# Kernel optimization log

Hardware: AMD Instinct MI355X
Metric: run time of the kernel (lower is better)

## Reference

```python
import jax, jax.numpy as jnp
import numpy as np

D = 128

def setup_inputs() -> dict:
    key = jax.random.key(0)
    k1, k2, k3, k4, k5, k6, k7 = jax.random.split(key, 7)
    B, L = 2048, 200
    target = jax.random.normal(k1, (B, D), dtype=jnp.float32)
    item_seq = jax.random.normal(k2, (B, L, D), dtype=jnp.float32)
    seq_len = jax.random.randint(k3, (B,), 0, 200, dtype=jnp.int64 if jax.config.jax_enable_x64 else jnp.int32)
    # MLP params: Linear(4D -> 2D), Linear(2D -> 1), PyTorch-style init scale
    s1 = 1.0 / np.sqrt(4 * D)
    s2 = 1.0 / np.sqrt(2 * D)
    W1 = jax.random.uniform(k4, (4 * D, 2 * D), minval=-s1, maxval=s1, dtype=jnp.float32)
    b1 = jax.random.uniform(k5, (2 * D,), minval=-s1, maxval=s1, dtype=jnp.float32)
    W2 = jax.random.uniform(k6, (2 * D, 1), minval=-s2, maxval=s2, dtype=jnp.float32)
    b2 = jax.random.uniform(k7, (1,), minval=-s2, maxval=s2, dtype=jnp.float32)
    return {"target": target, "item_seq": item_seq, "seq_len": seq_len,
            "W1": W1, "b1": b1, "W2": W2, "b2": b2}

def reference(target, item_seq, seq_len, W1, b1, W2, b2):
    B, L, Dd = item_seq.shape
    t = target[:, None, :]                              # B 1 D (broadcast over L)
    tgt = jnp.broadcast_to(t, (B, L, Dd))
    sub = item_seq - tgt
    dot = item_seq * tgt
    mlp_in = jnp.concatenate([tgt, item_seq, sub, dot], axis=-1)   # B L 4D
    h = jax.nn.relu(jnp.einsum('blf,fh->blh', mlp_in, W1) + b1)    # B L 2D
    score = jnp.einsum('blh,ho->blo', h, W2) + b2                  # B L 1
    mask = (jnp.arange(L)[None, :] < seq_len[:, None]).astype(item_seq.dtype)  # B L
    weighted = score * item_seq * mask[:, :, None]                 # B L D
    return jnp.sum(weighted, axis=1)                               # B D
```

## Files before the change

### kernel.cpp

```cpp
#include <hip/hip_runtime.h>
#include <hip/hip_bf16.h>

typedef short short8 __attribute__((ext_vector_type(8)));
typedef float f32x4 __attribute__((ext_vector_type(4)));

#define XS 136

static __device__ inline short f2bf(float f) {
    unsigned u = __float_as_uint(f);
    unsigned r = (u + 0x7fffu + ((u >> 16) & 1u)) >> 16;
    return (short)r;
}
static __device__ inline float bf2f(short s) {
    return __uint_as_float(((unsigned)(unsigned short)s) << 16);
}

__global__ void prep(const float* __restrict__ W1, short* __restrict__ Wbc,
                     short* __restrict__ Wd) {
    int idx = blockIdx.x * 256 + threadIdx.x;
    int half = idx >> 15;
    int i = idx & 32767;
    int j = i & 7;
    int l = (i >> 3) & 63;
    int s = (i >> 9) & 3;
    int t = i >> 11;
    int k = s * 32 + ((l >> 4) << 3) + j;
    int n = t * 16 + (l & 15);
    if (half == 0) Wbc[i] = f2bf(W1[(128 + k) * 256 + n] + W1[(256 + k) * 256 + n]);
    else           Wd[i]  = f2bf(W1[(384 + k) * 256 + n]);
}

__global__ void compute_u(const float* __restrict__ target, const float* __restrict__ W1,
                          const float* __restrict__ b1, float* __restrict__ U) {
    const int b8 = blockIdx.x;
    const int tid = threadIdx.x;
    __shared__ float tl[1024];
#pragma unroll
    for (int k = 0; k < 4; k++) tl[k * 256 + tid] = target[b8 * 1024 + k * 256 + tid];
    __syncthreads();
    float acc[8] = {0.f, 0.f, 0.f, 0.f, 0.f, 0.f, 0.f, 0.f};
#pragma unroll 8
    for (int d = 0; d < 128; ++d) {
        float wud = W1[d * 256 + tid] - W1[(256 + d) * 256 + tid];
#pragma unroll
        for (int r = 0; r < 8; r++) acc[r] += tl[r * 128 + d] * wud;
    }
    float bj = b1[tid];
#pragma unroll
    for (int r = 0; r < 8; r++) U[(b8 * 8 + r) * 256 + tid] = acc[r] + bj;
}

__launch_bounds__(256, 2)
__global__ void din_main(const float* __restrict__ target, const float* __restrict__ item_seq,
                         const int* __restrict__ seq_len, const float* __restrict__ W2,
                         const float* __restrict__ b2p, const short* __restrict__ Wbc,
                         const short* __restrict__ Wd, const float* __restrict__ U,
                         float* __restrict__ out) {
    const int b = blockIdx.x;
    const int tid = threadIdx.x;
    const int lane = tid & 63;
    const int w = tid >> 6;
    const int col = lane & 15;
    const int q = lane >> 4;

    const int slen = seq_len[b];
    const int nt = (slen + 15) >> 4;

    __shared__ __attribute__((aligned(16))) short Xl[2][16 * XS];
    __shared__ __attribute__((aligned(16))) float tsh[128];
    __shared__ float u_s[256];
    __shared__ float w2_s[256];
    __shared__ __attribute__((aligned(16))) float scoreP[16][4];
    __shared__ float out_s[128];

    const int r = tid >> 4;
    const int c = (tid & 15) << 3;

    float4 v0, v1;
    {
        const float4* src = (const float4*)(item_seq + (((size_t)b * 200 + r) * 128 + c));
        v0 = src[0]; v1 = src[1];
    }

    if (tid < 128) tsh[tid] = target[b * 128 + tid];
    u_s[tid] = U[b * 256 + tid];
    w2_s[tid] = W2[tid];
    const float b2 = b2p[0];
    __syncthreads();

    short8 bfrag[4][4];
#pragma unroll
    for (int s = 0; s < 4; s++) {
        const float4* tp = (const float4*)(tsh + s * 32 + q * 8);
        float4 ta = tp[0], tb = tp[1];
        float tk[8] = {ta.x, ta.y, ta.z, ta.w, tb.x, tb.y, tb.z, tb.w};
#pragma unroll
        for (int i = 0; i < 4; i++) {
            size_t off = ((size_t)((w * 4 + i) * 4 + s) * 64 + lane) * 8;
            short8 bc = *(const short8*)(Wbc + off);
            short8 dd = *(const short8*)(Wd + off);
            short8 e;
#pragma unroll
            for (int j = 0; j < 8; j++) e[j] = f2bf(bf2f(bc[j]) + tk[j] * bf2f(dd[j]));
            bfrag[i][s] = e;
        }
    }

    float u_c[4], w2c[4];
#pragma unroll
    for (int i = 0; i < 4; i++) {
        int j = (w * 4 + i) * 16 + col;
        u_c[i] = u_s[j];
        w2c[i] = w2_s[j];
    }

    const int d = tid & 127;
    const int g = tid >> 7;
    float out_val = 0.f;
    f32x4 acc[4];

    for (int mt = 0; mt < nt; ++mt) {
        const int l0 = mt * 16;
        short* xb = Xl[mt & 1];

        {
            float v[8] = {v0.x, v0.y, v0.z, v0.w, v1.x, v1.y, v1.z, v1.w};
            short8 p;
#pragma unroll
            for (int j = 0; j < 8; j++) p[j] = f2bf(v[j]);
            *(short8*)(xb + r * XS + c) = p;
        }
        __syncthreads();

        if (mt + 1 < nt) {
            int lr = l0 + 16 + r;
            if (lr > 199) lr = 199;
            const float4* src = (const float4*)(item_seq + (((size_t)b * 200 + lr) * 128 + c));
            v0 = src[0]; v1 = src[1];
        }

#pragma unroll
        for (int i = 0; i < 4; i++) acc[i] = (f32x4){0.f, 0.f, 0.f, 0.f};
        const short* arow = xb + col * XS + q * 8;
#pragma unroll
        for (int s = 0; s < 4; s++) {
            short8 af = *(const short8*)(arow + s * 32);
#pragma unroll
            for (int i = 0; i < 4; i++)
                acc[i] = __builtin_amdgcn_mfma_f32_16x16x32_bf16(af, bfrag[i][s], acc[i], 0, 0, 0);
        }

        float sv[4];
#pragma unroll
        for (int rg = 0; rg < 4; rg++) {
            float s0 = 0.f;
#pragma unroll
            for (int i = 0; i < 4; i++) {
                float h = acc[i][rg] + u_c[i];
                h = h > 0.f ? h : 0.f;
                s0 += h * w2c[i];
            }
            sv[rg] = s0;
        }
#pragma unroll
        for (int off = 1; off < 16; off <<= 1) {
#pragma unroll
            for (int rg = 0; rg < 4; rg++) sv[rg] += __shfl_xor(sv[rg], off, 64);
        }
        if (col == 0) {
#pragma unroll
            for (int rg = 0; rg < 4; rg++) scoreP[q * 4 + rg][w] = sv[rg];
        }
        __syncthreads();

#pragma unroll
        for (int mm = 0; mm < 8; mm++) {
            int m = g * 8 + mm;
            int l = l0 + m;
            float4 sp = *(const float4*)&scoreP[m][0];
            float s = (sp.x + sp.y) + (sp.z + sp.w) + b2;
            s = (l < slen) ? s : 0.f;
            out_val += s * bf2f(xb[m * XS + d]);
        }
    }

    __syncthreads();
    if (g == 1) out_s[d] = out_val;
    __syncthreads();
    if (g == 0) out[b * 128 + d] = out_val + out_s[d];
}

extern "C" void kernel_launch(void* const* d_in, const int* in_sizes, int n_in,
                              void* d_out, int out_size, void* d_ws, size_t ws_size,
                              hipStream_t stream) {
    const float* target   = (const float*)d_in[0];
    const float* item_seq = (const float*)d_in[1];
    const int*   seq_len  = (const int*)d_in[2];
    const float* W1       = (const float*)d_in[3];
    const float* b1       = (const float*)d_in[4];
    const float* W2       = (const float*)d_in[5];
    const float* b2       = (const float*)d_in[6];
    float* out = (float*)d_out;

    char* ws = (char*)d_ws;
    short* Wbc = (short*)ws;
    short* Wd  = (short*)(ws + 65536);
    float* U   = (float*)(ws + 131072);

    prep<<<256, 256, 0, stream>>>(W1, Wbc, Wd);
    compute_u<<<256, 256, 0, stream>>>(target, W1, b1, U);
    din_main<<<2048, 256, 0, stream>>>(target, item_seq, seq_len, W2, b2, Wbc, Wd, U, out);
}
```

Measured before the change: 312.3 us.

## Use persistent blocks with an atomic work counter for batch scheduling

Replaces the one-block-per-batch-row launch with 1024 persistent blocks that pull batch indices from a global atomic counter. The counter is reset in the prep kernel. The aim is to balance uneven per-row work, since sequence lengths vary, and to avoid tail imbalance and block launch overhead. In exchange it adds an atomic and an extra barrier per row, and it loses the prefetch overlap between rows because the first item_seq load now comes after claiming a row.

```diff
diff --git a/kernel.cpp b/kernel.cpp
--- a/kernel.cpp
+++ b/kernel.cpp
@@ -16,8 +16,9 @@
 }
 
 __global__ void prep(const float* __restrict__ W1, short* __restrict__ Wbc,
-                     short* __restrict__ Wd) {
+                     short* __restrict__ Wd, int* __restrict__ counter) {
     int idx = blockIdx.x * 256 + threadIdx.x;
+    if (idx == 0) *counter = 0;
     int half = idx >> 15;
     int i = idx & 32767;
     int j = i & 7;
@@ -55,139 +56,139 @@
                          const int* __restrict__ seq_len, const float* __restrict__ W2,
                          const float* __restrict__ b2p, const short* __restrict__ Wbc,
                          const short* __restrict__ Wd, const float* __restrict__ U,
-                         float* __restrict__ out) {
-    const int b = blockIdx.x;
+                         int* __restrict__ counter, float* __restrict__ out) {
     const int tid = threadIdx.x;
     const int lane = tid & 63;
     const int w = tid >> 6;
     const int col = lane & 15;
     const int q = lane >> 4;
-
-    const int slen = seq_len[b];
-    const int nt = (slen + 15) >> 4;
+    const int r = tid >> 4;
+    const int c = (tid & 15) << 3;
+    const int d = tid & 127;
+    const int g = tid >> 7;
 
     __shared__ __attribute__((aligned(16))) short Xl[2][16 * XS];
     __shared__ __attribute__((aligned(16))) float tsh[128];
-    __shared__ float u_s[256];
-    __shared__ float w2_s[256];
     __shared__ __attribute__((aligned(16))) float scoreP[16][4];
     __shared__ float out_s[128];
-
-    const int r = tid >> 4;
-    const int c = (tid & 15) << 3;
-
-    float4 v0, v1;
-    {
-        const float4* src = (const float4*)(item_seq + (((size_t)b * 200 + r) * 128 + c));
-        v0 = src[0]; v1 = src[1];
-    }
-
-    if (tid < 128) tsh[tid] = target[b * 128 + tid];
-    u_s[tid] = U[b * 256 + tid];
-    w2_s[tid] = W2[tid];
+    __shared__ int cur_b;
+
     const float b2 = b2p[0];
-    __syncthreads();
-
-    short8 bfrag[4][4];
-#pragma unroll
-    for (int s = 0; s < 4; s++) {
-        const float4* tp = (const float4*)(tsh + s * 32 + q * 8);
-        float4 ta = tp[0], tb = tp[1];
-        float tk[8] = {ta.x, ta.y, ta.z, ta.w, tb.x, tb.y, tb.z, tb.w};
-#pragma unroll
-        for (int i = 0; i < 4; i++) {
-            size_t off = ((size_t)((w * 4 + i) * 4 + s) * 64 + lane) * 8;
-            short8 bc = *(const short8*)(Wbc + off);
-            short8 dd = *(const short8*)(Wd + off);
-            short8 e;
-#pragma unroll
-            for (int j = 0; j < 8; j++) e[j] = f2bf(bf2f(bc[j]) + tk[j] * bf2f(dd[j]));
-            bfrag[i][s] = e;
-        }
-    }
-
-    float u_c[4], w2c[4];
-#pragma unroll
-    for (int i = 0; i < 4; i++) {
-        int j = (w * 4 + i) * 16 + col;
-        u_c[i] = u_s[j];
-        w2c[i] = w2_s[j];
-    }
-
-    const int d = tid & 127;
-    const int g = tid >> 7;
-    float out_val = 0.f;
-    f32x4 acc[4];
-
-    for (int mt = 0; mt < nt; ++mt) {
-        const int l0 = mt * 16;
-        short* xb = Xl[mt & 1];
-
+    float w2c[4];
+#pragma unroll
+    for (int i = 0; i < 4; i++) w2c[i] = W2[(w * 4 + i) * 16 + col];
+
+    for (;;) {
+        if (tid == 0) cur_b = atomicAdd(counter, 1);
+        __syncthreads();
+        const int b = cur_b;
+        if (b >= 2048) return;
+
+        const int slen = seq_len[b];
+        const int nt = (slen + 15) >> 4;
+
+        float4 v0, v1;
         {
-            float v[8] = {v0.x, v0.y, v0.z, v0.w, v1.x, v1.y, v1.z, v1.w};
-            short8 p;
-#pragma unroll
-            for (int j = 0; j < 8; j++) p[j] = f2bf(v[j]);
-            *(short8*)(xb + r * XS + c) = p;
-        }
-        __syncthreads();
-
-        if (mt + 1 < nt) {
-            int lr = l0 + 16 + r;
-            if (lr > 199) lr = 199;
-            const float4* src = (const float4*)(item_seq + (((size_t)b * 200 + lr) * 128 + c));
+            const float4* src = (const float4*)(item_seq + (((size_t)b * 200 + r) * 128 + c));
             v0 = src[0]; v1 = src[1];
         }
-
-#pragma unroll
-        for (int i = 0; i < 4; i++) acc[i] = (f32x4){0.f, 0.f, 0.f, 0.f};
-        const short* arow = xb + col * XS + q * 8;
+        float u_c[4];
+#pragma unroll
+        for (int i = 0; i < 4; i++) u_c[i] = U[b * 256 + (w * 4 + i) * 16 + col];
+        if (tid < 128) tsh[tid] = target[b * 128 + tid];
+        __syncthreads();
+
+        short8 bfrag[4][4];
 #pragma unroll
         for (int s = 0; s < 4; s++) {
-            short8 af = *(const short8*)(arow + s * 32);
-#pragma unroll
-            for (int i = 0; i < 4; i++)
-                acc[i] = __builtin_amdgcn_mfma_f32_16x16x32_bf16(af, bfrag[i][s], acc[i], 0, 0, 0);
+            const float4* tp = (const float4*)(tsh + s * 32 + q * 8);
+            float4 ta = tp[0], tb = tp[1];
+            float tk[8] = {ta.x, ta.y, ta.z, ta.w, tb.x, tb.y, tb.z, tb.w};
+#pragma unroll
+            for (int i = 0; i < 4; i++) {
+                size_t off = ((size_t)((w * 4 + i) * 4 + s) * 64 + lane) * 8;
+                short8 bc = *(const short8*)(Wbc + off);
+                short8 dd = *(const short8*)(Wd + off);
+                short8 e;
+#pragma unroll
+                for (int j = 0; j < 8; j++) e[j] = f2bf(bf2f(bc[j]) + tk[j] * bf2f(dd[j]));
+                bfrag[i][s] = e;
+            }
         }
 
-        float sv[4];
-#pragma unroll
-        for (int rg = 0; rg < 4; rg++) {
-            float s0 = 0.f;
-#pragma unroll
-            for (int i = 0; i < 4; i++) {
-                float h = acc[i][rg] + u_c[i];
-                h = h > 0.f ? h : 0.f;
-                s0 += h * w2c[i];
-            }
-            sv[rg] = s0;
+        float out_val = 0.f;
+        f32x4 acc[4];
+
+        for (int mt = 0; mt < nt; ++mt) {
+            const int l0 = mt * 16;
+            short* xb = Xl[mt & 1];
+
+            {
+                float v[8] = {v0.x, v0.y, v0.z, v0.w, v1.x, v1.y, v1.z, v1.w};
+                short8 p;
+#pragma unroll
+                for (int j = 0; j < 8; j++) p[j] = f2bf(v[j]);
+                *(short8*)(xb + r * XS + c) = p;
+            }
+            __syncthreads();
+
+            if (mt + 1 < nt) {
+                int lr = l0 + 16 + r;
+                if (lr > 199) lr = 199;
+                const float4* src = (const float4*)(item_seq + (((size_t)b * 200 + lr) * 128 + c));
+                v0 = src[0]; v1 = src[1];
+            }
+
+#pragma unroll
+            for (int i = 0; i < 4; i++) acc[i] = (f32x4){0.f, 0.f, 0.f, 0.f};
+            const short* arow = xb + col * XS + q * 8;
+#pragma unroll
+            for (int s = 0; s < 4; s++) {
+                short8 af = *(const short8*)(arow + s * 32);
+#pragma unroll
+                for (int i = 0; i < 4; i++)
+                    acc[i] = __builtin_amdgcn_mfma_f32_16x16x32_bf16(af, bfrag[i][s], acc[i], 0, 0, 0);
+            }
+
+            float sv[4];
+#pragma unroll
+            for (int rg = 0; rg < 4; rg++) {
+                float s0 = 0.f;
+#pragma unroll
+                for (int i = 0; i < 4; i++) {
+                    float h = acc[i][rg] + u_c[i];
+                    h = h > 0.f ? h : 0.f;
+                    s0 += h * w2c[i];
+                }
+                sv[rg] = s0;
+            }
+#pragma unroll
+            for (int off = 1; off < 16; off <<= 1) {
+#pragma unroll
+                for (int rg = 0; rg < 4; rg++) sv[rg] += __shfl_xor(sv[rg], off, 64);
+            }
+            if (col == 0) {
+#pragma unroll
+                for (int rg = 0; rg < 4; rg++) scoreP[q * 4 + rg][w] = sv[rg];
+            }
+            __syncthreads();
+
+#pragma unroll
+            for (int mm = 0; mm < 8; mm++) {
+                int m = g * 8 + mm;
+                int l = l0 + m;
+                float4 sp = *(const float4*)&scoreP[m][0];
+                float s = (sp.x + sp.y) + (sp.z + sp.w) + b2;
+                s = (l < slen) ? s : 0.f;
+                out_val += s * bf2f(xb[m * XS + d]);
+            }
         }
-#pragma unroll
-        for (int off = 1; off < 16; off <<= 1) {
-#pragma unroll
-            for (int rg = 0; rg < 4; rg++) sv[rg] += __shfl_xor(sv[rg], off, 64);
-        }
-        if (col == 0) {
-#pragma unroll
-            for (int rg = 0; rg < 4; rg++) scoreP[q * 4 + rg][w] = sv[rg];
-        }
-        __syncthreads();
-
-#pragma unroll
-        for (int mm = 0; mm < 8; mm++) {
-            int m = g * 8 + mm;
-            int l = l0 + m;
-            float4 sp = *(const float4*)&scoreP[m][0];
-            float s = (sp.x + sp.y) + (sp.z + sp.w) + b2;
-            s = (l < slen) ? s : 0.f;
-            out_val += s * bf2f(xb[m * XS + d]);
-        }
+
+        __syncthreads();
+        if (g == 1) out_s[d] = out_val;
+        __syncthreads();
+        if (g == 0) out[b * 128 + d] = out_val + out_s[d];
     }
-
-    __syncthreads();
-    if (g == 1) out_s[d] = out_val;
-    __syncthreads();
-    if (g == 0) out[b * 128 + d] = out_val + out_s[d];
 }
 
 extern "C" void kernel_launch(void* const* d_in, const int* in_sizes, int n_in,
@@ -203,11 +204,12 @@
     float* out = (float*)d_out;
 
     char* ws = (char*)d_ws;
-    short* Wbc = (short*)ws;
-    short* Wd  = (short*)(ws + 65536);
-    float* U   = (float*)(ws + 131072);
-
-    prep<<<256, 256, 0, stream>>>(W1, Wbc, Wd);
+    short* Wbc   = (short*)ws;
+    short* Wd    = (short*)(ws + 65536);
+    float* U     = (float*)(ws + 131072);
+    int* counter = (int*)(ws + 131072 + 2097152);
+
+    prep<<<256, 256, 0, stream>>>(W1, Wbc, Wd, counter);
     compute_u<<<256, 256, 0, stream>>>(target, W1, b1, U);
-    din_main<<<2048, 256, 0, stream>>>(target, item_seq, seq_len, W2, b2, Wbc, Wd, U, out);
-}
+    din_main<<<1024, 256, 0, stream>>>(target, item_seq, seq_len, W2, b2, Wbc, Wd, U, counter, out);
+}
```

Result: no change. 313.8 us (+0.5%).
